# Kernel tuning notes

Hardware: AMD Instinct MI355X
Metric: run time of the kernel (lower is better)

Reference implementation:

```python
import jax, jax.numpy as jnp
from jax import lax
import numpy as np

PATCH = 16
FREQ = 8
TWO_PI = 2.0 * np.pi


def setup_inputs() -> dict:
    key = jax.random.key(0)
    ks = jax.random.split(key, 4)
    B, C, H, W = 8, 64, 128, 128
    E, O, HID = 8, 64, 128
    GATE_C = C + 4 * FREQ  # 96
    x = jax.random.normal(ks[0], (B, C, H, W), dtype=jnp.float32)
    We = jax.random.normal(ks[1], (E, O, C, 3, 3), dtype=jnp.float32) * (1.0 / np.sqrt(C * 9))
    be = jnp.zeros((E, O), dtype=jnp.float32)
    W1 = jax.random.normal(ks[2], (HID, GATE_C), dtype=jnp.float32) * (1.0 / np.sqrt(GATE_C))
    b1 = jnp.zeros((HID,), dtype=jnp.float32)
    W2 = jax.random.normal(ks[3], (E, HID), dtype=jnp.float32) * (1.0 / np.sqrt(HID))
    b2 = jnp.zeros((E,), dtype=jnp.float32)
    return {"x": x, "We": We, "be": be, "W1": W1, "b1": b1, "W2": W2, "b2": b2}


def _fourier_grid(nH, nW, dtype):
    # positional Fourier features of patch centers: [4*FREQ, nH, nW]
    u = (jnp.arange(nH, dtype=dtype) + 0.5) / nH
    v = (jnp.arange(nW, dtype=dtype) + 0.5) / nW
    uu, vv = jnp.meshgrid(u, v, indexing="ij")  # [nH,nW]
    freqs = (2.0 ** jnp.arange(FREQ, dtype=dtype))[:, None, None]
    au = TWO_PI * freqs * uu[None]
    av = TWO_PI * freqs * vv[None]
    return jnp.concatenate([jnp.sin(au), jnp.cos(au), jnp.sin(av), jnp.cos(av)], axis=0)


def reference(x, We, be, W1, b1, W2, b2):
    B, C, H, W = x.shape
    E = We.shape[0]
    P = PATCH
    nH, nW = H // P, W // P

    # --- router gate: per-patch pooled channels + fourier positional feats ---
    xp = x.reshape(B, C, nH, P, nW, P).mean(axis=(3, 5))  # [B,C,nH,nW]
    four = _fourier_grid(nH, nW, x.dtype)  # [4F,nH,nW]
    g = jnp.concatenate([xp, jnp.broadcast_to(four, (B,) + four.shape)], axis=1)  # [B,gate_c,nH,nW]
    h = jax.nn.relu(jnp.einsum("hc,bcij->bhij", W1, g) + b1[None, :, None, None])
    logits = jnp.einsum("eh,bhij->beij", W2, h) + b2[None, :, None, None]
    probs = jax.nn.softmax(logits, axis=1)  # [B,E,nH,nW]

    # --- conv experts (3x3, SAME, ReLU; dropout inactive at eval) ---
    def expert(w, b):
        y = lax.conv_general_dilated(x, w, (1, 1), "SAME",
                                     dimension_numbers=("NCHW", "OIHW", "NCHW"))
        return jax.nn.relu(y + b[None, :, None, None])

    y = jax.vmap(expert)(We, be)  # [E,B,O,H,W]

    # --- combine: broadcast patch gates to pixels and weight-sum experts ---
    gates = jnp.repeat(jnp.repeat(probs, P, axis=2), P, axis=3)  # [B,E,H,W]
    out = jnp.einsum("ebchw,behw->bchw", y, gates)
    return out
```

## Files before the change

### kernel.cpp

```cpp
#include <hip/hip_runtime.h>
#include <math.h>

#define BB 8
#define CC 64
#define HH 128
#define WW 128
#define EE 8
#define OO 64
#define HID 128
#define GATEC 96
#define NP 8
#define PP 16

typedef __attribute__((ext_vector_type(8))) short bf16x8;
typedef __attribute__((ext_vector_type(4))) float f32x4;

static __device__ __forceinline__ unsigned short f2bf(float f) {
  unsigned int u = __builtin_bit_cast(unsigned int, f);
  unsigned int r = (u + 0x7FFFu + ((u >> 16) & 1u)) >> 16;
  return (unsigned short)r;
}

static __device__ __forceinline__ void gll16(const void* g, void* l) {
  __builtin_amdgcn_global_load_lds(
      (const __attribute__((address_space(1))) void*)g,
      (__attribute__((address_space(3))) void*)l, 16, 0, 0);
}

__global__ __launch_bounds__(256) void gate_kernel(
    const float* __restrict__ x,
    const float* __restrict__ W1, const float* __restrict__ b1,
    const float* __restrict__ W2, const float* __restrict__ b2,
    float* __restrict__ probs) {
  int blk = blockIdx.x;
  int b  = blk >> 6;
  int pi = (blk >> 3) & 7;
  int pj = blk & 7;
  int t  = threadIdx.x;

  __shared__ float ps[256];
  __shared__ float g[GATEC];
  __shared__ float hbuf[HID];
  __shared__ float lg[EE];

  {
    int c = t >> 2, q = t & 3;
    const float* xb = x + ((size_t)(b * CC + c) * HH + pi * PP + q * 4) * WW + pj * PP;
    float s = 0.f;
    for (int r = 0; r < 4; ++r)
      for (int col = 0; col < PP; ++col)
        s += xb[r * WW + col];
    ps[t] = s;
  }
  __syncthreads();
  if (t < CC) {
    g[t] = (ps[4*t] + ps[4*t+1] + ps[4*t+2] + ps[4*t+3]) * (1.f / 256.f);
  } else if (t < CC + 32) {
    int k = t - CC;
    int fi = k & 7, kind = k >> 3;
    float freq  = (float)(1 << fi);
    float coord = (kind < 2) ? ((pi + 0.5f) / 8.f) : ((pj + 0.5f) / 8.f);
    float a = 6.28318530717958647692f * freq * coord;
    g[t] = (kind & 1) ? cosf(a) : sinf(a);
  }
  __syncthreads();
  if (t < HID) {
    float acc = b1[t];
    const float* w = W1 + (size_t)t * GATEC;
    for (int c = 0; c < GATEC; ++c) acc += w[c] * g[c];
    hbuf[t] = fmaxf(acc, 0.f);
  }
  __syncthreads();
  if (t < EE) {
    float acc = b2[t];
    const float* w = W2 + (size_t)t * HID;
    for (int k = 0; k < HID; ++k) acc += w[k] * hbuf[k];
    lg[t] = acc;
  }
  __syncthreads();
  if (t < EE) {
    float m = lg[0];
    for (int e = 1; e < EE; ++e) m = fmaxf(m, lg[e]);
    float sum = 0.f;
    for (int e = 0; e < EE; ++e) sum += expf(lg[e] - m);
    probs[((size_t)(b * EE + t) * NP + pi) * NP + pj] = expf(lg[t] - m) / sum;
  }
}

__global__ __launch_bounds__(256) void pack_kernel(
    const float* __restrict__ We, unsigned short* __restrict__ wp) {
  int idx = blockIdx.x * 256 + threadIdx.x;
  if (idx >= EE * 9 * OO * CC) return;
  int c  = idx & 63;
  int o  = (idx >> 6) & 63;
  int et = idx >> 12;
  int t  = et % 9;
  int e  = et / 9;
  float v = We[(((size_t)(e * OO + o) * CC) + c) * 9 + t];
  int dst = (et << 12) + (o << 6) + ((((c >> 3) ^ (o & 7)) << 3) | (c & 7));
  wp[dst] = f2bf(v);
}

__global__ __launch_bounds__(256, 2) void conv_moe(
    const float* __restrict__ x,
    const unsigned short* __restrict__ wp,
    const float* __restrict__ be,
    const float* __restrict__ probs, float* __restrict__ out) {
  int bx0 = blockIdx.x;
  int b   = blockIdx.y;
  int rg = bx0 >> 2, cg = bx0 & 3;
  const int h0 = rg * 8, w0 = cg * 32;
  const int pi = rg >> 1;
  const int pj0 = cg * 2;

  int lane = threadIdx.x & 63;
  int wave = threadIdx.x >> 6;
  int px   = lane & 15;
  int kg   = lane >> 4;

  __shared__ char xs[340 * 128];
  __shared__ char wb[2][16384];

  for (int idx = threadIdx.x; idx < 340 * 8; idx += 256) {
    int j  = idx / 340;
    int sp = idx % 340;
    int r = sp / 34, col = sp % 34;
    int gr = h0 + r - 1, gc = w0 + col - 1;
    bf16x8 v;
    if (gr >= 0 && gr < HH && gc >= 0 && gc < WW) {
      const float* xb = x + ((size_t)(b * CC + j * 8) * HH + gr) * WW + gc;
#pragma unroll
      for (int q = 0; q < 8; ++q) v[q] = (short)f2bf(xb[(size_t)q * HH * WW]);
    } else {
#pragma unroll
      for (int q = 0; q < 8; ++q) v[q] = 0;
    }
    int g = (gr + gc) & 7;
    *(bf16x8*)(xs + sp * 128 + ((j ^ g) & 7) * 16) = v;
  }

  {
    const char* src = (const char*)wp + (size_t)(wave * 4) * 1024 + lane * 16;
    char* dst = &wb[0][(wave * 4) * 1024];
#pragma unroll
    for (int i = 0; i < 4; ++i)
      gll16(src + i * 1024, dst + i * 1024);
  }
  __syncthreads();

  f32x4 outacc[4][4], acc[4][4];
#pragma unroll
  for (int ot = 0; ot < 4; ++ot)
#pragma unroll
    for (int f = 0; f < 4; ++f) { outacc[ot][f] = (f32x4)(0.f); acc[ot][f] = (f32x4)(0.f); }

  const int gl = h0 + w0 - 2 + wave * 2 + px;

  int t9 = 0, dy = 0, dx = 0, e = 0;
  for (int u = 0; u < 36; ++u) {
    int cur = u & 1;
    if (u < 35) {
      const char* src = (const char*)wp + (size_t)(u + 1) * 16384 + (wave * 4) * 1024 + lane * 16;
      char* dst = &wb[cur ^ 1][(wave * 4) * 1024];
#pragma unroll
      for (int i = 0; i < 4; ++i)
        gll16(src + i * 1024, dst + i * 1024);
    }
#pragma unroll
    for (int ht = 0; ht < 2; ++ht) {
      const char* wt = &wb[cur][ht * 8192];
#pragma unroll
      for (int ks = 0; ks < 2; ++ks) {
        bf16x8 aw[4], bxv[4];
#pragma unroll
        for (int ot = 0; ot < 4; ++ot)
          aw[ot] = *(const bf16x8*)(wt + (ot * 16 + px) * 128 +
                                    ((((ks << 2) | kg) ^ (px & 7)) << 4));
#pragma unroll
        for (int f = 0; f < 4; ++f) {
          int rowp = f >> 1, ch = f & 1;
          int sp = (wave * 2 + rowp + dy) * 34 + ch * 16 + px + dx;
          int g  = (gl + rowp + dy + dx) & 7;
          bxv[f] = *(const bf16x8*)(xs + sp * 128 + (((((ks << 2) | kg) ^ g) & 7) << 4));
        }
#pragma unroll
        for (int ot = 0; ot < 4; ++ot)
#pragma unroll
          for (int f = 0; f < 4; ++f)
            acc[ot][f] = __builtin_amdgcn_mfma_f32_16x16x32_bf16(
                aw[ot], bxv[f], acc[ot][f], 0, 0, 0);
      }
      if (++dx == 3) { dx = 0; ++dy; }
      if (++t9 == 9) {
        float gA = probs[((size_t)(b * EE + e) * NP + pi) * NP + pj0];
        float gB = probs[((size_t)(b * EE + e) * NP + pi) * NP + pj0 + 1];
#pragma unroll
        for (int ot = 0; ot < 4; ++ot) {
          f32x4 bias = *(const f32x4*)(be + e * OO + ot * 16 + kg * 4);
#pragma unroll
          for (int f = 0; f < 4; ++f) {
            float gt = (f & 1) ? gB : gA;
#pragma unroll
            for (int r = 0; r < 4; ++r) {
              outacc[ot][f][r] += gt * fmaxf(acc[ot][f][r] + bias[r], 0.f);
              acc[ot][f][r] = 0.f;
            }
          }
        }
        t9 = 0; dy = 0; dx = 0; ++e;
      }
    }
    __syncthreads();
  }

#pragma unroll
  for (int ot = 0; ot < 4; ++ot) {
#pragma unroll
    for (int f = 0; f < 4; ++f) {
      int rowp = f >> 1, ch = f & 1;
      int o = ot * 16 + kg * 4;
      int h = h0 + wave * 2 + rowp;
      float* op = out + ((size_t)(b * OO + o) * HH + h) * WW + w0 + ch * 16 + px;
#pragma unroll
      for (int r = 0; r < 4; ++r)
        op[(size_t)r * HH * WW] = outacc[ot][f][r];
    }
  }
}

extern "C" void kernel_launch(void* const* d_in, const int* in_sizes, int n_in,
                              void* d_out, int out_size, void* d_ws, size_t ws_size,
                              hipStream_t stream) {
  const float* x  = (const float*)d_in[0];
  const float* We = (const float*)d_in[1];
  const float* be = (const float*)d_in[2];
  const float* W1 = (const float*)d_in[3];
  const float* b1 = (const float*)d_in[4];
  const float* W2 = (const float*)d_in[5];
  const float* b2 = (const float*)d_in[6];
  float* out = (float*)d_out;

  float* probs = (float*)d_ws;
  unsigned short* wpk = (unsigned short*)((char*)d_ws + 16384);

  gate_kernel<<<dim3(BB * NP * NP), dim3(256), 0, stream>>>(x, W1, b1, W2, b2, probs);
  pack_kernel<<<dim3((EE * 9 * OO * CC + 255) / 256), dim3(256), 0, stream>>>(We, wpk);
  conv_moe<<<dim3(16 * 4, BB), dim3(256), 0, stream>>>(x, wpk, be, probs, out);
}
```

Measured before the change: 103.7 us.

## Merge gate and pack kernels, software-pipeline LDS loads with MFMA in conv loop

Folds the gate and weight-pack kernels into one launch, using a block-index split, so one kernel launch is removed. The first weight-tile async load is issued before the input tile staging so the two overlap. The inner loop is restructured into double-buffered register fragments: the next fragments are loaded from LDS while MFMAs run, with s_setprio raising wave priority around MFMA bursts. This raises register pressure, which could hurt occupancy at launch bounds of 2 blocks.

```diff
diff --git a/kernel.cpp b/kernel.cpp
--- a/kernel.cpp
+++ b/kernel.cpp
@@ -27,21 +27,37 @@
       (__attribute__((address_space(3))) void*)l, 16, 0, 0);
 }
 
-__global__ __launch_bounds__(256) void gate_kernel(
+__global__ __launch_bounds__(256) void prep_kernel(
     const float* __restrict__ x,
     const float* __restrict__ W1, const float* __restrict__ b1,
     const float* __restrict__ W2, const float* __restrict__ b2,
-    float* __restrict__ probs) {
+    const float* __restrict__ We,
+    float* __restrict__ probs, unsigned short* __restrict__ wp) {
+  __shared__ float ps[256];
+  __shared__ float g[GATEC];
+  __shared__ float hbuf[HID];
+  __shared__ float lg[EE];
+
+  if (blockIdx.x >= 512) {
+    int idx = (blockIdx.x - 512) * 256 + threadIdx.x;
+    if (idx < EE * 9 * OO * CC) {
+      int c  = idx & 63;
+      int o  = (idx >> 6) & 63;
+      int et = idx >> 12;
+      int t  = et % 9;
+      int e  = et / 9;
+      float v = We[(((size_t)(e * OO + o) * CC) + c) * 9 + t];
+      int dst = (et << 12) + (o << 6) + ((((c >> 3) ^ (o & 7)) << 3) | (c & 7));
+      wp[dst] = f2bf(v);
+    }
+    return;
+  }
+
   int blk = blockIdx.x;
   int b  = blk >> 6;
   int pi = (blk >> 3) & 7;
   int pj = blk & 7;
   int t  = threadIdx.x;
-
-  __shared__ float ps[256];
-  __shared__ float g[GATEC];
-  __shared__ float hbuf[HID];
-  __shared__ float lg[EE];
 
   {
     int c = t >> 2, q = t & 3;
@@ -85,20 +101,6 @@
     for (int e = 0; e < EE; ++e) sum += expf(lg[e] - m);
     probs[((size_t)(b * EE + t) * NP + pi) * NP + pj] = expf(lg[t] - m) / sum;
   }
-}
-
-__global__ __launch_bounds__(256) void pack_kernel(
-    const float* __restrict__ We, unsigned short* __restrict__ wp) {
-  int idx = blockIdx.x * 256 + threadIdx.x;
-  if (idx >= EE * 9 * OO * CC) return;
-  int c  = idx & 63;
-  int o  = (idx >> 6) & 63;
-  int et = idx >> 12;
-  int t  = et % 9;
-  int e  = et / 9;
-  float v = We[(((size_t)(e * OO + o) * CC) + c) * 9 + t];
-  int dst = (et << 12) + (o << 6) + ((((c >> 3) ^ (o & 7)) << 3) | (c & 7));
-  wp[dst] = f2bf(v);
 }
 
 __global__ __launch_bounds__(256, 2) void conv_moe(
@@ -121,6 +123,14 @@
   __shared__ char xs[340 * 128];
   __shared__ char wb[2][16384];
 
+  {
+    const char* src = (const char*)wp + (size_t)(wave * 4) * 1024 + lane * 16;
+    char* dst = &wb[0][(wave * 4) * 1024];
+#pragma unroll
+    for (int i = 0; i < 4; ++i)
+      gll16(src + i * 1024, dst + i * 1024);
+  }
+
   for (int idx = threadIdx.x; idx < 340 * 8; idx += 256) {
     int j  = idx / 340;
     int sp = idx % 340;
@@ -138,14 +148,6 @@
     int g = (gr + gc) & 7;
     *(bf16x8*)(xs + sp * 128 + ((j ^ g) & 7) * 16) = v;
   }
-
-  {
-    const char* src = (const char*)wp + (size_t)(wave * 4) * 1024 + lane * 16;
-    char* dst = &wb[0][(wave * 4) * 1024];
-#pragma unroll
-    for (int i = 0; i < 4; ++i)
-      gll16(src + i * 1024, dst + i * 1024);
-  }
   __syncthreads();
 
   f32x4 outacc[4][4], acc[4][4];
@@ -156,7 +158,59 @@
 
   const int gl = h0 + w0 - 2 + wave * 2 + px;
 
-  int t9 = 0, dy = 0, dx = 0, e = 0;
+#define LOADAW(dst, wt, ks)                                                     \
+  {                                                                             \
+    _Pragma("unroll")                                                           \
+    for (int ot = 0; ot < 4; ++ot)                                              \
+      dst[ot] = *(const bf16x8*)((wt) + (ot * 16 + px) * 128 +                  \
+                                 (((((ks) << 2) | kg) ^ (px & 7)) << 4));       \
+  }
+
+#define LOADBX(dst, dy, dx, ks)                                                 \
+  {                                                                             \
+    _Pragma("unroll")                                                           \
+    for (int f = 0; f < 4; ++f) {                                               \
+      int rowp = f >> 1, ch = f & 1;                                            \
+      int sp = (wave * 2 + rowp + (dy)) * 34 + ch * 16 + px + (dx);             \
+      int slot = (((((ks) << 2) | kg) ^ (gl + rowp + (dy) + (dx))) & 7);        \
+      dst[f] = *(const bf16x8*)(xs + sp * 128 + (slot << 4));                   \
+    }                                                                           \
+  }
+
+#define MFMA16(A, B)                                                            \
+  {                                                                             \
+    __builtin_amdgcn_s_setprio(1);                                              \
+    _Pragma("unroll")                                                           \
+    for (int ot = 0; ot < 4; ++ot)                                              \
+      _Pragma("unroll")                                                         \
+      for (int f = 0; f < 4; ++f)                                               \
+        acc[ot][f] = __builtin_amdgcn_mfma_f32_16x16x32_bf16(A[ot], B[f],       \
+                                                             acc[ot][f], 0, 0, 0); \
+    __builtin_amdgcn_s_setprio(0);                                              \
+  }
+
+#define EPILOGUE(eidx)                                                          \
+  {                                                                             \
+    float gA = probs[((size_t)(b * EE + (eidx)) * NP + pi) * NP + pj0];         \
+    float gB = probs[((size_t)(b * EE + (eidx)) * NP + pi) * NP + pj0 + 1];     \
+    _Pragma("unroll")                                                           \
+    for (int ot = 0; ot < 4; ++ot) {                                            \
+      f32x4 bias = *(const f32x4*)(be + (eidx) * OO + ot * 16 + kg * 4);        \
+      _Pragma("unroll")                                                         \
+      for (int f = 0; f < 4; ++f) {                                             \
+        float gt = (f & 1) ? gB : gA;                                           \
+        _Pragma("unroll")                                                       \
+        for (int r = 0; r < 4; ++r) {                                           \
+          outacc[ot][f][r] += gt * fmaxf(acc[ot][f][r] + bias[r], 0.f);         \
+          acc[ot][f][r] = 0.f;                                                  \
+        }                                                                       \
+      }                                                                         \
+    }                                                                           \
+  }
+
+  bf16x8 A0[4], B0[4], A1[4], B1[4];
+  int e = 0, t9A = 0, dyA = 0, dxA = 0;
+
   for (int u = 0; u < 36; ++u) {
     int cur = u & 1;
     if (u < 35) {
@@ -166,50 +220,26 @@
       for (int i = 0; i < 4; ++i)
         gll16(src + i * 1024, dst + i * 1024);
     }
-#pragma unroll
-    for (int ht = 0; ht < 2; ++ht) {
-      const char* wt = &wb[cur][ht * 8192];
-#pragma unroll
-      for (int ks = 0; ks < 2; ++ks) {
-        bf16x8 aw[4], bxv[4];
-#pragma unroll
-        for (int ot = 0; ot < 4; ++ot)
-          aw[ot] = *(const bf16x8*)(wt + (ot * 16 + px) * 128 +
-                                    ((((ks << 2) | kg) ^ (px & 7)) << 4));
-#pragma unroll
-        for (int f = 0; f < 4; ++f) {
-          int rowp = f >> 1, ch = f & 1;
-          int sp = (wave * 2 + rowp + dy) * 34 + ch * 16 + px + dx;
-          int g  = (gl + rowp + dy + dx) & 7;
-          bxv[f] = *(const bf16x8*)(xs + sp * 128 + (((((ks << 2) | kg) ^ g) & 7) << 4));
-        }
-#pragma unroll
-        for (int ot = 0; ot < 4; ++ot)
-#pragma unroll
-          for (int f = 0; f < 4; ++f)
-            acc[ot][f] = __builtin_amdgcn_mfma_f32_16x16x32_bf16(
-                aw[ot], bxv[f], acc[ot][f], 0, 0, 0);
-      }
-      if (++dx == 3) { dx = 0; ++dy; }
-      if (++t9 == 9) {
-        float gA = probs[((size_t)(b * EE + e) * NP + pi) * NP + pj0];
-        float gB = probs[((size_t)(b * EE + e) * NP + pi) * NP + pj0 + 1];
-#pragma unroll
-        for (int ot = 0; ot < 4; ++ot) {
-          f32x4 bias = *(const f32x4*)(be + e * OO + ot * 16 + kg * 4);
-#pragma unroll
-          for (int f = 0; f < 4; ++f) {
-            float gt = (f & 1) ? gB : gA;
-#pragma unroll
-            for (int r = 0; r < 4; ++r) {
-              outacc[ot][f][r] += gt * fmaxf(acc[ot][f][r] + bias[r], 0.f);
-              acc[ot][f][r] = 0.f;
-            }
-          }
-        }
-        t9 = 0; dy = 0; dx = 0; ++e;
-      }
-    }
+    int t9B = t9A + 1, dyB = dyA, dxB = dxA + 1;
+    if (dxB == 3) { dxB = 0; dyB += 1; }
+    if (t9B == 9) { t9B = 0; dyB = 0; dxB = 0; }
+    const char* wtA = &wb[cur][0];
+    const char* wtB = &wb[cur][8192];
+
+    LOADAW(A0, wtA, 0); LOADBX(B0, dyA, dxA, 0);
+    LOADAW(A1, wtA, 1); LOADBX(B1, dyA, dxA, 1);
+    MFMA16(A0, B0);
+    LOADAW(A0, wtB, 0); LOADBX(B0, dyB, dxB, 0);
+    MFMA16(A1, B1);
+    if (t9A == 8) { EPILOGUE(e); ++e; }
+    LOADAW(A1, wtB, 1); LOADBX(B1, dyB, dxB, 1);
+    MFMA16(A0, B0);
+    MFMA16(A1, B1);
+    if (t9B == 8) { EPILOGUE(e); ++e; }
+
+    t9A = t9B + 1; dyA = dyB; dxA = dxB + 1;
+    if (dxA == 3) { dxA = 0; dyA += 1; }
+    if (t9A == 9) { t9A = 0; dyA = 0; dxA = 0; }
     __syncthreads();
   }
 
@@ -226,6 +256,10 @@
         op[(size_t)r * HH * WW] = outacc[ot][f][r];
     }
   }
+#undef LOADAW
+#undef LOADBX
+#undef MFMA16
+#undef EPILOGUE
 }
 
 extern "C" void kernel_launch(void* const* d_in, const int* in_sizes, int n_in,
@@ -243,7 +277,7 @@
   float* probs = (float*)d_ws;
   unsigned short* wpk = (unsigned short*)((char*)d_ws + 16384);
 
-  gate_kernel<<<dim3(BB * NP * NP), dim3(256), 0, stream>>>(x, W1, b1, W2, b2, probs);
-  pack_kernel<<<dim3((EE * 9 * OO * CC + 255) / 256), dim3(256), 0, stream>>>(We, wpk);
+  prep_kernel<<<dim3(512 + (EE * 9 * OO * CC + 255) / 256), dim3(256), 0, stream>>>(
+      x, W1, b1, W2, b2, We, probs, wpk);
   conv_moe<<<dim3(16 * 4, BB), dim3(256), 0, stream>>>(x, wpk, be, probs, out);
 }
```

New measurement: 103.1 us. No clear change (-0.6%).
